# Kernel tuning notes

Measured on AMD Instinct MI355X. Metric: run time of the kernel, lower is better.

The kernel has to match this reference:

```python
import jax, jax.numpy as jnp
import numpy as np

N, E, F_IN, NUM_GRAPHS, K = 50000, 500000, 160, 128, 3


def _glorot(k, shape):
    lim = np.sqrt(6.0 / (shape[-2] + shape[-1])).astype(np.float32)
    return jax.random.uniform(k, shape, jnp.float32, -lim, lim)


def setup_inputs() -> dict:
    key = jax.random.key(0)
    ks = jax.random.split(key, 8)
    x = jax.random.normal(ks[0], (N, F_IN), jnp.float32)
    edge_index = jax.random.randint(ks[1], (2, E), 0, N)
    edge_attr = jax.random.uniform(ks[2], (E,), jnp.float32)
    batch = jnp.sort(jax.random.randint(ks[3], (N,), 0, NUM_GRAPHS))
    W1 = _glorot(ks[4], (K, F_IN, 128)); b1 = jnp.zeros((128,), jnp.float32)
    W2 = _glorot(ks[5], (K, 128, 64)); b2 = jnp.zeros((64,), jnp.float32)
    W3 = _glorot(ks[6], (K, 64, 32)); b3 = jnp.zeros((32,), jnp.float32)
    Wl = _glorot(ks[7], (32, 2)); bl = jnp.zeros((2,), jnp.float32)
    return dict(x=x, edge_index=edge_index, edge_attr=edge_attr, batch=batch,
                W1=W1, b1=b1, W2=W2, b2=b2, W3=W3, b3=b3, Wl=Wl, bl=bl)


def _cheb_norm(src, dst, edge_attr, n):
    # PyG ChebConv: sym-normalized Laplacian, lambda_max=2 =>
    # L_hat = (2/lmax)*L_sym - I = -D^{-1/2} A D^{-1/2} (diagonal = 0)
    deg = jax.ops.segment_sum(edge_attr, src, num_segments=n)
    safe = jnp.where(deg > 0, deg, 1.0)
    dinv = jnp.where(deg > 0, jax.lax.rsqrt(safe), 0.0)
    return -dinv[src] * edge_attr * dinv[dst]


def _propagate(x, src, dst, w, n):
    # out[dst] += w * x[src]  (sparse L_hat @ x)
    return jax.ops.segment_sum(w[:, None] * x[src], dst, num_segments=n)


def _cheb_conv(x, src, dst, w, W, b, n):
    # Chebyshev recurrence: T0 = x, T1 = L_hat x, Tk = 2 L_hat T(k-1) - T(k-2)
    tx0 = x
    out = tx0 @ W[0]
    tx1 = _propagate(tx0, src, dst, w, n)
    out = out + tx1 @ W[1]
    for k in range(2, W.shape[0]):
        tx2 = 2.0 * _propagate(tx1, src, dst, w, n) - tx0
        out = out + tx2 @ W[k]
        tx0, tx1 = tx1, tx2
    return out + b


def reference(x, edge_index, edge_attr, batch, W1, b1, W2, b2, W3, b3, Wl, bl):
    n = x.shape[0]
    src, dst = edge_index[0], edge_index[1]
    w = _cheb_norm(src, dst, edge_attr, n)
    h = jax.nn.relu(_cheb_conv(x, src, dst, w, W1, b1, n))
    h = jax.nn.relu(_cheb_conv(h, src, dst, w, W2, b2, n))
    h = jax.nn.relu(_cheb_conv(h, src, dst, w, W3, b3, n))
    # global_mean_pool over graph ids (dropout omitted: eval mode)
    sums = jax.ops.segment_sum(h, batch, num_segments=NUM_GRAPHS)
    cnt = jax.ops.segment_sum(jnp.ones((n,), h.dtype), batch, num_segments=NUM_GRAPHS)
    pooled = sums / jnp.maximum(cnt, 1.0)[:, None]
    return pooled @ Wl + bl
```

## Files before the change

### kernel.cpp

```cpp
#include <hip/hip_runtime.h>

#define N_NODES 50000
#define N_EDGES 500000
#define NUM_G   128
#define SCAN_NB 49
#define PN      (SCAN_NB * 1024)
#define NCX     32
#define NCX_SH  5
#define ECH     15628
#define RNG     8192
#define NRY     7
#define HVB     (2 * NCX * NRY)
#define WPREPB  360
#define RNG_SC  2688
#define NRY_SC  19
#define SCVB    (NCX * NRY_SC)
#define GEMM_MB 782

typedef __attribute__((ext_vector_type(8))) short short8;
typedef __attribute__((ext_vector_type(4))) float f32x4;
typedef __attribute__((ext_vector_type(2))) float f32x2;

__device__ __forceinline__ unsigned f2bf(float x) {
    unsigned u = __float_as_uint(x);
    return (u + 0x7FFFu + ((u >> 16) & 1u)) >> 16;
}
__device__ __forceinline__ float bf2f(unsigned h) {
    return __uint_as_float(h << 16);
}

__device__ __forceinline__ void wprep_one(const float* __restrict__ W, unsigned short* __restrict__ WT,
                                          int t, int FIN, int F) {
    int n = t / FIN, k = t - n * FIN;
    int sel = n / F, c = n - sel * F;
    float v;
    if (sel == 0) v = W[(size_t)k * F + c] - W[(size_t)2 * FIN * F + (size_t)k * F + c];
    else          v = W[(size_t)sel * FIN * F + (size_t)k * F + c];
    WT[t] = (unsigned short)f2bf(v);
}

__global__ __launch_bounds__(256)
void prep_kernel(const int* __restrict__ src, const int* __restrict__ dst,
                 const float* __restrict__ ea,
                 float* __restrict__ pdeg, int* __restrict__ pcnt,
                 const float* __restrict__ W1, const float* __restrict__ W2,
                 const float* __restrict__ W3,
                 unsigned short* __restrict__ WT1, unsigned short* __restrict__ WT2,
                 unsigned short* __restrict__ WT3) {
    __shared__ unsigned lh[RNG];
    int vb = blockIdx.x, tid = threadIdx.x;
    if (vb < HVB) {
        bool isdeg = vb < NCX * NRY;
        int v2 = isdeg ? vb : vb - NCX * NRY;
        int xk = v2 & (NCX - 1), y = v2 >> NCX_SH;
        int base = y * RNG;
        for (int i = tid; i < RNG; i += 256) lh[i] = 0u;
        __syncthreads();
        int e0 = xk * ECH, e1 = min(e0 + ECH, N_EDGES);
        if (isdeg) {
            for (int e = e0 + tid * 4; e < e1; e += 1024) {
                int4 s4 = *reinterpret_cast<const int4*>(src + e);
                if ((unsigned)(s4.x - base) < RNG) atomicAdd((float*)&lh[s4.x - base], ea[e]);
                if ((unsigned)(s4.y - base) < RNG) atomicAdd((float*)&lh[s4.y - base], ea[e + 1]);
                if ((unsigned)(s4.z - base) < RNG) atomicAdd((float*)&lh[s4.z - base], ea[e + 2]);
                if ((unsigned)(s4.w - base) < RNG) atomicAdd((float*)&lh[s4.w - base], ea[e + 3]);
            }
        } else {
            for (int e = e0 + tid * 4; e < e1; e += 1024) {
                int4 d4 = *reinterpret_cast<const int4*>(dst + e);
                if ((unsigned)(d4.x - base) < RNG) atomicAdd((int*)&lh[d4.x - base], 1);
                if ((unsigned)(d4.y - base) < RNG) atomicAdd((int*)&lh[d4.y - base], 1);
                if ((unsigned)(d4.z - base) < RNG) atomicAdd((int*)&lh[d4.z - base], 1);
                if ((unsigned)(d4.w - base) < RNG) atomicAdd((int*)&lh[d4.w - base], 1);
            }
        }
        __syncthreads();
        if (isdeg) {
            for (int i = tid; i < RNG; i += 256) {
                int n = base + i;
                if (n < PN) pdeg[(size_t)xk * PN + n] = ((float*)lh)[i];
            }
        } else {
            for (int i = tid; i < RNG; i += 256) {
                int n = base + i;
                if (n < PN) pcnt[(size_t)xk * PN + n] = ((int*)lh)[i];
            }
        }
    } else {
        int t = (vb - HVB) * 256 + tid;
        if (t < 61440)      wprep_one(W1, WT1, t, 160, 128);
        else if (t < 86016) wprep_one(W2, WT2, t - 61440, 128, 64);
        else if (t < 92160) wprep_one(W3, WT3, t - 86016, 64, 32);
    }
}

__global__ __launch_bounds__(256)
void reduce_scan_kernel(const float* __restrict__ pdeg, int* __restrict__ pcnt,
                        float* __restrict__ dinv, int* __restrict__ cnt,
                        int* __restrict__ partial) {
    int b = blockIdx.x, t = threadIdx.x;
    int i0 = b * 1024 + t * 4;
    float d0 = 0.f, d1 = 0.f, d2 = 0.f, d3 = 0.f;
    int r0 = 0, r1 = 0, r2 = 0, r3 = 0;
    for (int x = 0; x < NCX; ++x) {
        float4 pv = *reinterpret_cast<const float4*>(pdeg + (size_t)x * PN + i0);
        int4   cv = *reinterpret_cast<const int4*>(pcnt + (size_t)x * PN + i0);
        *reinterpret_cast<int4*>(pcnt + (size_t)x * PN + i0) = make_int4(r0, r1, r2, r3);
        d0 += pv.x; d1 += pv.y; d2 += pv.z; d3 += pv.w;
        r0 += cv.x; r1 += cv.y; r2 += cv.z; r3 += cv.w;
    }
    float dd[4] = {d0, d1, d2, d3};
    int   rr[4] = {r0, r1, r2, r3};
    int s = 0;
    #pragma unroll
    for (int j = 0; j < 4; ++j) {
        int n = i0 + j;
        if (n < N_NODES) {
            float dv = dd[j], r = 0.f;
            if (dv > 0.f) {
                r = rsqrtf(dv);
                r = r * (1.5f - 0.5f * dv * r * r);
            }
            dinv[n] = r;
            cnt[n] = rr[j];
            s += rr[j];
        } else {
            cnt[n] = 0;
        }
    }
    __shared__ int red[256];
    red[t] = s;
    __syncthreads();
    for (int off = 128; off > 0; off >>= 1) {
        if (t < off) red[t] += red[t + off];
        __syncthreads();
    }
    if (t == 0) partial[b] = red[0];
}

__global__ __launch_bounds__(256)
void scan_final_kernel(const int* __restrict__ cnt, const int* __restrict__ partial,
                       int* __restrict__ rowptr, int n) {
    int b = blockIdx.x, t = threadIdx.x;
    __shared__ int red[256];
    __shared__ int sh_off, sh_tot;
    if (t < 64) {
        int orig = (t < SCAN_NB) ? partial[t] : 0;
        int v = orig;
        #pragma unroll
        for (int off = 1; off < 64; off <<= 1) {
            int u = __shfl_up(v, off, 64);
            if (t >= off) v += u;
        }
        if (t == b) sh_off = v - orig;
        if (t == SCAN_NB - 1) sh_tot = v;
    }
    __syncthreads();
    int4 v = reinterpret_cast<const int4*>(cnt)[b * 256 + t];
    int s = v.x + v.y + v.z + v.w;
    red[t] = s;
    __syncthreads();
    for (int off = 1; off < 256; off <<= 1) {
        int u = (t >= off) ? red[t - off] : 0;
        __syncthreads();
        red[t] += u;
        __syncthreads();
    }
    int excl = sh_off + ((t == 0) ? 0 : red[t - 1]);
    int i0 = b * 1024 + t * 4;
    if (i0 < n)     rowptr[i0]     = excl;
    if (i0 + 1 < n) rowptr[i0 + 1] = excl + v.x;
    if (i0 + 2 < n) rowptr[i0 + 2] = excl + v.x + v.y;
    if (i0 + 3 < n) rowptr[i0 + 3] = excl + v.x + v.y + v.z;
    if (b == SCAN_NB - 1 && t == 0) rowptr[n] = sh_tot;
}

__device__ void scatter_body(int vb, const int* __restrict__ src, const int* __restrict__ dst,
                             const float* __restrict__ ea,
                             const int* __restrict__ rowptr, const int* __restrict__ pcnt,
                             int2* __restrict__ csr, unsigned char* smraw) {
    int* cursor = (int*)smraw;
    int tid = threadIdx.x;
    int x = vb & (NCX - 1), y = vb >> NCX_SH;
    int base = y * RNG_SC;
    for (int i = tid; i < RNG_SC; i += 256) {
        int n = base + i;
        cursor[i] = (n < N_NODES) ? (rowptr[n] + pcnt[(size_t)x * PN + n]) : 0;
    }
    __syncthreads();
    int e0 = x * ECH, e1 = min(e0 + ECH, N_EDGES);
    for (int e = e0 + tid * 4; e < e1; e += 1024) {
        int4 d4 = *reinterpret_cast<const int4*>(dst + e);
        if ((unsigned)(d4.x - base) < RNG_SC) {
            int pos = atomicAdd(&cursor[d4.x - base], 1);
            csr[pos] = make_int2(src[e], __float_as_int(ea[e]));
        }
        if ((unsigned)(d4.y - base) < RNG_SC) {
            int pos = atomicAdd(&cursor[d4.y - base], 1);
            csr[pos] = make_int2(src[e + 1], __float_as_int(ea[e + 1]));
        }
        if ((unsigned)(d4.z - base) < RNG_SC) {
            int pos = atomicAdd(&cursor[d4.z - base], 1);
            csr[pos] = make_int2(src[e + 2], __float_as_int(ea[e + 2]));
        }
        if ((unsigned)(d4.w - base) < RNG_SC) {
            int pos = atomicAdd(&cursor[d4.w - base], 1);
            csr[pos] = make_int2(src[e + 3], __float_as_int(ea[e + 3]));
        }
    }
}

template<int FIN, int F, bool AFP32>
__device__ void gemm_body(int bx, const void* __restrict__ Araw,
                          const unsigned short* __restrict__ WT, const float* __restrict__ dinv,
                          unsigned short* __restrict__ Y0, unsigned short* __restrict__ Y1,
                          unsigned short* __restrict__ Y2, int nrows, unsigned char* smraw) {
    constexpr int KT = FIN / 32;
    constexpr int NT = F / 32;
    constexpr int NTT = 3 * NT;
    constexpr int SA = FIN + 8;
    constexpr int F8 = FIN / 8;
    short* Bs = (short*)smraw;

    int tid = threadIdx.x;
    int lane = tid & 63, w = tid >> 6;
    int m0 = bx * 64;

    int colb = lane & 15;
    int q8 = (lane >> 4) << 3;
    int rq = (lane >> 4) << 2;
    int arow = m0 + w * 16 + colb;
    bool rok = arow < nrows;

    short8 afr[KT];
    #pragma unroll
    for (int kt = 0; kt < KT; ++kt) {
        short8 z = {0, 0, 0, 0, 0, 0, 0, 0};
        if (!rok) { afr[kt] = z; continue; }
        if constexpr (AFP32) {
            const float* A = (const float*)Araw;
            float4 f0 = *reinterpret_cast<const float4*>(A + (size_t)arow * FIN + (kt << 5) + q8);
            float4 f1 = *reinterpret_cast<const float4*>(A + (size_t)arow * FIN + (kt << 5) + q8 + 4);
            short8 r;
            r[0] = (short)f2bf(f0.x); r[1] = (short)f2bf(f0.y);
            r[2] = (short)f2bf(f0.z); r[3] = (short)f2bf(f0.w);
            r[4] = (short)f2bf(f1.x); r[5] = (short)f2bf(f1.y);
            r[6] = (short)f2bf(f1.z); r[7] = (short)f2bf(f1.w);
            afr[kt] = r;
        } else {
            const unsigned short* A = (const unsigned short*)Araw;
            afr[kt] = *reinterpret_cast<const short8*>(A + (size_t)arow * FIN + (kt << 5) + q8);
        }
    }

    for (int nt = 0; nt < NTT; ++nt) {
        int n0 = nt << 5;
        __syncthreads();
        for (int span = tid; span < 32 * F8; span += 256) {
            int r = span / F8, c8 = (span - r * F8) << 3;
            int pr = (r < 16) ? (r << 1) : (((r - 16) << 1) + 1);
            *reinterpret_cast<uint4*>(&Bs[r * SA + c8]) =
                *reinterpret_cast<const uint4*>(WT + (size_t)(n0 + pr) * FIN + c8);
        }
        __syncthreads();

        f32x4 acc0 = {0.f, 0.f, 0.f, 0.f}, acc1 = acc0;
        #pragma unroll
        for (int kt = 0; kt < KT; ++kt) {
            short8 b0 = *reinterpret_cast<const short8*>(&Bs[colb * SA + (kt << 5) + q8]);
            short8 b1 = *reinterpret_cast<const short8*>(&Bs[(colb + 16) * SA + (kt << 5) + q8]);
            acc0 = __builtin_amdgcn_mfma_f32_16x16x32_bf16(afr[kt], b0, acc0, 0, 0, 0);
            acc1 = __builtin_amdgcn_mfma_f32_16x16x32_bf16(afr[kt], b1, acc1, 0, 0, 0);
        }

        int g = nt / NT;
        int ntg = nt - g * NT;
        unsigned short* Ys = (g == 0) ? Y0 : (g == 1) ? Y1 : Y2;
        int lc = (ntg << 5) + (colb << 1);
        #pragma unroll
        for (int r = 0; r < 4; ++r) {
            int orow = m0 + w * 16 + rq + r;
            if (orow < nrows) {
                float sc = (g == 2) ? dinv[orow] : 1.0f;
                unsigned pack = f2bf(acc0[r] * sc) | (f2bf(acc1[r] * sc) << 16);
                *reinterpret_cast<unsigned*>(Ys + (size_t)orow * F + lc) = pack;
            }
        }
    }
}

__global__ __launch_bounds__(256)
void sg_kernel(const int* __restrict__ src, const int* __restrict__ dst,
               const float* __restrict__ ea,
               const int* __restrict__ rowptr, const int* __restrict__ pcnt,
               int2* __restrict__ csr,
               const float* __restrict__ x, const unsigned short* __restrict__ WT1,
               const float* __restrict__ dinv,
               unsigned short* __restrict__ Y0, unsigned short* __restrict__ Y1,
               unsigned short* __restrict__ Y2) {
    __shared__ alignas(16) unsigned char sm[32 * (160 + 8) * 2];
    int vb = blockIdx.x;
    if (vb < SCVB) {
        scatter_body(vb, src, dst, ea, rowptr, pcnt, csr, sm);
    } else {
        gemm_body<160, 128, true>(vb - SCVB, x, WT1, dinv, Y0, Y1, Y2, N_NODES, sm);
    }
}

template<int FIN, int F>
__launch_bounds__(256)
__global__ void cheb_gemm(const unsigned short* __restrict__ Xb, const unsigned short* __restrict__ WT,
                          const float* __restrict__ dinv,
                          unsigned short* __restrict__ Y0, unsigned short* __restrict__ Y1,
                          unsigned short* __restrict__ Y2, int nrows) {
    __shared__ alignas(16) unsigned char sm[32 * (FIN + 8) * 2];
    gemm_body<FIN, F, false>(blockIdx.x, Xb, WT, dinv, Y0, Y1, Y2, nrows, sm);
}

__device__ __forceinline__ void acc8p(f32x2* acc, uint4 p, float wv) {
    f32x2 w2; w2[0] = wv; w2[1] = wv;
    f32x2 a0, a1, a2, a3;
    a0[0] = __uint_as_float(p.x << 16); a0[1] = __uint_as_float(p.x & 0xFFFF0000u);
    a1[0] = __uint_as_float(p.y << 16); a1[1] = __uint_as_float(p.y & 0xFFFF0000u);
    a2[0] = __uint_as_float(p.z << 16); a2[1] = __uint_as_float(p.z & 0xFFFF0000u);
    a3[0] = __uint_as_float(p.w << 16); a3[1] = __uint_as_float(p.w & 0xFFFF0000u);
    acc[0] += w2 * a0;
    acc[1] += w2 * a1;
    acc[2] += w2 * a2;
    acc[3] += w2 * a3;
}

__device__ __forceinline__ void expand8(uint4 p, float* o) {
    o[0] = bf2f(p.x & 0xFFFFu);
    o[1] = __uint_as_float(p.x & 0xFFFF0000u);
    o[2] = bf2f(p.y & 0xFFFFu);
    o[3] = __uint_as_float(p.y & 0xFFFF0000u);
    o[4] = bf2f(p.z & 0xFFFFu);
    o[5] = __uint_as_float(p.z & 0xFFFF0000u);
    o[6] = bf2f(p.w & 0xFFFFu);
    o[7] = __uint_as_float(p.w & 0xFFFF0000u);
}

template<int F, int MODE>
__launch_bounds__(256)
__global__ void gather_kernel(const unsigned short* __restrict__ X, const int2* __restrict__ csr,
                              const int* __restrict__ rowptr, const float* __restrict__ dinv,
                              const unsigned short* __restrict__ Y, const float* __restrict__ bias,
                              unsigned short* __restrict__ O, int n) {
    constexpr int FQ8 = F >> 3;
    constexpr int DPB = 256 / FQ8;
    constexpr int CAP = 1280;
    __shared__ int2 scsr[CAP];
    __shared__ int srp[DPB + 1];
    __shared__ int smap[DPB];
    int tid = threadIdx.x;
    int db0 = blockIdx.x * DPB;
    if (tid <= DPB) srp[tid] = rowptr[min(db0 + tid, n)];
    __syncthreads();
    int ebeg = srp[0];
    int ecnt = srp[DPB] - ebeg;
    bool staged = ecnt <= CAP;
    if (tid < DPB) {
        int my = srp[tid + 1] - srp[tid];
        int rk = 0;
        for (int g2 = 0; g2 < DPB; ++g2) {
            int l2 = srp[g2 + 1] - srp[g2];
            rk += (l2 < my) || (l2 == my && g2 < tid);
        }
        smap[rk] = tid;
    }
    if (staged) {
        for (int i = tid; i < ecnt; i += 256)
            scsr[i] = csr[ebeg + i];
    }
    __syncthreads();

    int gq = tid / FQ8;
    int rr = smap[gq];
    int d = db0 + rr;
    if (d >= n) return;
    int f8 = (tid - gq * FQ8) << 3;
    f32x2 acc[4];
    #pragma unroll
    for (int j = 0; j < 4; ++j) { acc[j][0] = 0.f; acc[j][1] = 0.f; }

    if (staged) {
        int beg = srp[rr] - ebeg, end = srp[rr + 1] - ebeg;
        int last = end - 1;
        for (int i = beg; i < end; i += 8) {
            int2 e0 = scsr[i];
            int2 e1 = scsr[min(i + 1, last)];
            int2 e2 = scsr[min(i + 2, last)];
            int2 e3 = scsr[min(i + 3, last)];
            int2 e4 = scsr[min(i + 4, last)];
            int2 e5 = scsr[min(i + 5, last)];
            int2 e6 = scsr[min(i + 6, last)];
            int2 e7 = scsr[min(i + 7, last)];
            uint4 p0 = *reinterpret_cast<const uint4*>(X + (size_t)e0.x * F + f8);
            uint4 p1 = *reinterpret_cast<const uint4*>(X + (size_t)e1.x * F + f8);
            uint4 p2 = *reinterpret_cast<const uint4*>(X + (size_t)e2.x * F + f8);
            uint4 p3 = *reinterpret_cast<const uint4*>(X + (size_t)e3.x * F + f8);
            uint4 p4 = *reinterpret_cast<const uint4*>(X + (size_t)e4.x * F + f8);
            uint4 p5 = *reinterpret_cast<const uint4*>(X + (size_t)e5.x * F + f8);
            uint4 p6 = *reinterpret_cast<const uint4*>(X + (size_t)e6.x * F + f8);
            uint4 p7 = *reinterpret_cast<const uint4*>(X + (size_t)e7.x * F + f8);
            float w0 = __int_as_float(e0.y);
            float w1 = (i + 1 < end) ? __int_as_float(e1.y) : 0.f;
            float w2 = (i + 2 < end) ? __int_as_float(e2.y) : 0.f;
            float w3 = (i + 3 < end) ? __int_as_float(e3.y) : 0.f;
            float w4 = (i + 4 < end) ? __int_as_float(e4.y) : 0.f;
            float w5 = (i + 5 < end) ? __int_as_float(e5.y) : 0.f;
            float w6 = (i + 6 < end) ? __int_as_float(e6.y) : 0.f;
            float w7 = (i + 7 < end) ? __int_as_float(e7.y) : 0.f;
            acc8p(acc, p0, w0);
            acc8p(acc, p1, w1);
            acc8p(acc, p2, w2);
            acc8p(acc, p3, w3);
            acc8p(acc, p4, w4);
            acc8p(acc, p5, w5);
            acc8p(acc, p6, w6);
            acc8p(acc, p7, w7);
        }
    } else {
        int beg = srp[rr], end = srp[rr + 1];
        for (int i = beg; i < end; ++i) {
            int2 e = csr[i];
            uint4 p = *reinterpret_cast<const uint4*>(X + (size_t)e.x * F + f8);
            acc8p(acc, p, __int_as_float(e.y));
        }
    }

    float accs[8];
    #pragma unroll
    for (int j = 0; j < 8; ++j) accs[j] = acc[j >> 1][j & 1];

    float y[8];
    expand8(*reinterpret_cast<const uint4*>(Y + (size_t)d * F + f8), y);
    float dv = dinv[d];
    float v[8];
    if (MODE == 0) {
        float dv2 = 2.f * dv;
        #pragma unroll
        for (int j = 0; j < 8; ++j) v[j] = dv * (y[j] - dv2 * accs[j]);
    } else {
        float4 ba = *reinterpret_cast<const float4*>(bias + f8);
        float4 bb = *reinterpret_cast<const float4*>(bias + f8 + 4);
        v[0] = fmaxf(y[0] - dv * accs[0] + ba.x, 0.f);
        v[1] = fmaxf(y[1] - dv * accs[1] + ba.y, 0.f);
        v[2] = fmaxf(y[2] - dv * accs[2] + ba.z, 0.f);
        v[3] = fmaxf(y[3] - dv * accs[3] + ba.w, 0.f);
        v[4] = fmaxf(y[4] - dv * accs[4] + bb.x, 0.f);
        v[5] = fmaxf(y[5] - dv * accs[5] + bb.y, 0.f);
        v[6] = fmaxf(y[6] - dv * accs[6] + bb.z, 0.f);
        v[7] = fmaxf(y[7] - dv * accs[7] + bb.w, 0.f);
    }
    uint4 o;
    o.x = f2bf(v[0]) | (f2bf(v[1]) << 16);
    o.y = f2bf(v[2]) | (f2bf(v[3]) << 16);
    o.z = f2bf(v[4]) | (f2bf(v[5]) << 16);
    o.w = f2bf(v[6]) | (f2bf(v[7]) << 16);
    *reinterpret_cast<uint4*>(O + (size_t)d * F + f8) = o;
}

__device__ __forceinline__ int lower_bound_dev(const int* __restrict__ a, int n, int v) {
    int lo = 0, hi = n;
    while (lo < hi) {
        int mid = (lo + hi) >> 1;
        if (a[mid] < v) lo = mid + 1; else hi = mid;
    }
    return lo;
}

__global__ void pool_kernel(const unsigned short* __restrict__ H, const int* __restrict__ batch,
                            const float* __restrict__ Wl, const float* __restrict__ bl,
                            float* __restrict__ out, int n) {
    int g = blockIdx.x;
    int start = lower_bound_dev(batch, n, g);
    int end   = lower_bound_dev(batch, n, g + 1);
    int tid = threadIdx.x;
    int f = tid & 31;
    int sub = tid >> 5;
    float acc = 0.0f;
    for (int i = start + sub; i < end; i += 8)
        acc += bf2f((unsigned)H[(size_t)i * 32 + f]);
    __shared__ float red[256];
    red[tid] = acc;
    __syncthreads();
    if (tid < 128) red[tid] += red[tid + 128];
    __syncthreads();
    if (tid < 64) red[tid] += red[tid + 64];
    __syncthreads();
    if (tid < 32) red[tid] += red[tid + 32];
    __syncthreads();
    if (tid < 2) {
        int cnt = end - start;
        float inv = 1.0f / (float)(cnt > 0 ? cnt : 1);
        float o = bl[tid];
        for (int f2 = 0; f2 < 32; ++f2)
            o += red[f2] * inv * Wl[f2 * 2 + tid];
        out[g * 2 + tid] = o;
    }
}

extern "C" void kernel_launch(void* const* d_in, const int* in_sizes, int n_in,
                              void* d_out, int out_size, void* d_ws, size_t ws_size,
                              hipStream_t stream) {
    const float* x     = (const float*)d_in[0];
    const int*   ei    = (const int*)d_in[1];
    const float* ea    = (const float*)d_in[2];
    const int*   batch = (const int*)d_in[3];
    const float* W1 = (const float*)d_in[4];
    const float* b1 = (const float*)d_in[5];
    const float* W2 = (const float*)d_in[6];
    const float* b2 = (const float*)d_in[7];
    const float* W3 = (const float*)d_in[8];
    const float* b3 = (const float*)d_in[9];
    const float* Wl = (const float*)d_in[10];
    const float* bl = (const float*)d_in[11];
    float* out = (float*)d_out;
    char* ws = (char*)d_ws;

    const int* src = ei;
    const int* dst = ei + N_EDGES;

    size_t off = 0;
    auto alloc = [&](size_t bytes) { char* p = ws + off; off += (bytes + 255) & ~(size_t)255; return p; };
    float* pdeg    = (float*)alloc((size_t)NCX * PN * 4);
    int*   pcnt    = (int*)  alloc((size_t)NCX * PN * 4);
    float* dinv    = (float*)alloc(N_NODES * 4);
    int*   cnt     = (int*)  alloc((size_t)PN * 4);
    int*   partial = (int*)  alloc(SCAN_NB * 4);
    int*   rowptr  = (int*)  alloc((N_NODES + 1) * 4);
    int2*  csr     = (int2*) alloc((size_t)N_EDGES * 8);
    unsigned short* Xb  = (unsigned short*)alloc((size_t)N_NODES * 160 * 2);
    unsigned short* Y0  = (unsigned short*)alloc((size_t)N_NODES * 128 * 2);
    unsigned short* Y1  = (unsigned short*)alloc((size_t)N_NODES * 128 * 2);
    unsigned short* Y2  = (unsigned short*)alloc((size_t)N_NODES * 128 * 2);
    unsigned short* U   = (unsigned short*)alloc((size_t)N_NODES * 128 * 2);
    unsigned short* WT1 = (unsigned short*)alloc((size_t)384 * 160 * 2);
    unsigned short* WT2 = (unsigned short*)alloc((size_t)192 * 128 * 2);
    unsigned short* WT3 = (unsigned short*)alloc((size_t)96 * 64 * 2);

    const int BT = 256;

    prep_kernel<<<HVB + WPREPB, BT, 0, stream>>>(src, dst, ea, pdeg, pcnt,
                                                 W1, W2, W3, WT1, WT2, WT3);
    reduce_scan_kernel<<<SCAN_NB, BT, 0, stream>>>(pdeg, pcnt, dinv, cnt, partial);
    scan_final_kernel<<<SCAN_NB, BT, 0, stream>>>(cnt, partial, rowptr, N_NODES);
    sg_kernel<<<SCVB + GEMM_MB, BT, 0, stream>>>(src, dst, ea, rowptr, pcnt, csr,
                                                 x, WT1, dinv, Y0, Y1, Y2);

    auto gb = [&](int F) { int DPB = 256 / (F / 8); return (N_NODES + DPB - 1) / DPB; };

    gather_kernel<128, 0><<<gb(128), BT, 0, stream>>>(Y2, csr, rowptr, dinv, Y1, nullptr, U, N_NODES);
    gather_kernel<128, 1><<<gb(128), BT, 0, stream>>>(U, csr, rowptr, dinv, Y0, b1, Xb, N_NODES);

    cheb_gemm<128, 64><<<GEMM_MB, BT, 0, stream>>>(Xb, WT2, dinv, Y0, Y1, Y2, N_NODES);
    gather_kernel<64, 0><<<gb(64), BT, 0, stream>>>(Y2, csr, rowptr, dinv, Y1, nullptr, U, N_NODES);
    gather_kernel<64, 1><<<gb(64), BT, 0, stream>>>(U, csr, rowptr, dinv, Y0, b2, Xb, N_NODES);

    cheb_gemm<64, 32><<<GEMM_MB, BT, 0, stream>>>(Xb, WT3, dinv, Y0, Y1, Y2, N_NODES);
    gather_kernel<32, 0><<<gb(32), BT, 0, stream>>>(Y2, csr, rowptr, dinv, Y1, nullptr, U, N_NODES);
    gather_kernel<32, 1><<<gb(32), BT, 0, stream>>>(U, csr, rowptr, dinv, Y0, b3, Xb, N_NODES);

    pool_kernel<<<NUM_G, BT, 0, stream>>>(Xb, batch, Wl, bl, out, N_NODES);
}
```

Baseline: 288.8 us.

## Split each destination row's edge list across two thread groups in gather kernel

The gather kernel now assigns two thread groups per destination node, each summing half of that node's incoming edges. The partial sums are combined through shared memory after a block barrier, and the staged CSR capacity shrinks to match the halved nodes per block. The aim is more memory-level parallelism and shorter per-thread dependency chains on the random row loads, at the cost of an extra barrier, shared-memory traffic and twice as many blocks. The histogram range and per-block count constants in the prep stage are also retuned.

```diff
diff --git a/kernel.cpp b/kernel.cpp
--- a/kernel.cpp
+++ b/kernel.cpp
@@ -8,8 +8,8 @@
 #define NCX     32
 #define NCX_SH  5
 #define ECH     15628
-#define RNG     8192
-#define NRY     7
+#define RNG     15360
+#define NRY     4
 #define HVB     (2 * NCX * NRY)
 #define WPREPB  360
 #define RNG_SC  2688
@@ -348,11 +348,13 @@
                               const unsigned short* __restrict__ Y, const float* __restrict__ bias,
                               unsigned short* __restrict__ O, int n) {
     constexpr int FQ8 = F >> 3;
-    constexpr int DPB = 256 / FQ8;
-    constexpr int CAP = 1280;
+    constexpr int TPR = 2 * FQ8;
+    constexpr int DPB = 256 / TPR;
+    constexpr int CAP = 768;
     __shared__ int2 scsr[CAP];
     __shared__ int srp[DPB + 1];
     __shared__ int smap[DPB];
+    __shared__ float comb[DPB * F];
     int tid = threadIdx.x;
     int db0 = blockIdx.x * DPB;
     if (tid <= DPB) srp[tid] = rowptr[min(db0 + tid, n)];
@@ -375,64 +377,82 @@
     }
     __syncthreads();
 
-    int gq = tid / FQ8;
+    int gq = tid / TPR;
+    int q  = tid - gq * TPR;
+    int sub = q / FQ8;
+    int fidx = q - sub * FQ8;
     int rr = smap[gq];
     int d = db0 + rr;
-    if (d >= n) return;
-    int f8 = (tid - gq * FQ8) << 3;
+    bool act = d < n;
+    int f8 = fidx << 3;
     f32x2 acc[4];
     #pragma unroll
     for (int j = 0; j < 4; ++j) { acc[j][0] = 0.f; acc[j][1] = 0.f; }
 
-    if (staged) {
-        int beg = srp[rr] - ebeg, end = srp[rr + 1] - ebeg;
-        int last = end - 1;
-        for (int i = beg; i < end; i += 8) {
-            int2 e0 = scsr[i];
-            int2 e1 = scsr[min(i + 1, last)];
-            int2 e2 = scsr[min(i + 2, last)];
-            int2 e3 = scsr[min(i + 3, last)];
-            int2 e4 = scsr[min(i + 4, last)];
-            int2 e5 = scsr[min(i + 5, last)];
-            int2 e6 = scsr[min(i + 6, last)];
-            int2 e7 = scsr[min(i + 7, last)];
-            uint4 p0 = *reinterpret_cast<const uint4*>(X + (size_t)e0.x * F + f8);
-            uint4 p1 = *reinterpret_cast<const uint4*>(X + (size_t)e1.x * F + f8);
-            uint4 p2 = *reinterpret_cast<const uint4*>(X + (size_t)e2.x * F + f8);
-            uint4 p3 = *reinterpret_cast<const uint4*>(X + (size_t)e3.x * F + f8);
-            uint4 p4 = *reinterpret_cast<const uint4*>(X + (size_t)e4.x * F + f8);
-            uint4 p5 = *reinterpret_cast<const uint4*>(X + (size_t)e5.x * F + f8);
-            uint4 p6 = *reinterpret_cast<const uint4*>(X + (size_t)e6.x * F + f8);
-            uint4 p7 = *reinterpret_cast<const uint4*>(X + (size_t)e7.x * F + f8);
-            float w0 = __int_as_float(e0.y);
-            float w1 = (i + 1 < end) ? __int_as_float(e1.y) : 0.f;
-            float w2 = (i + 2 < end) ? __int_as_float(e2.y) : 0.f;
-            float w3 = (i + 3 < end) ? __int_as_float(e3.y) : 0.f;
-            float w4 = (i + 4 < end) ? __int_as_float(e4.y) : 0.f;
-            float w5 = (i + 5 < end) ? __int_as_float(e5.y) : 0.f;
-            float w6 = (i + 6 < end) ? __int_as_float(e6.y) : 0.f;
-            float w7 = (i + 7 < end) ? __int_as_float(e7.y) : 0.f;
-            acc8p(acc, p0, w0);
-            acc8p(acc, p1, w1);
-            acc8p(acc, p2, w2);
-            acc8p(acc, p3, w3);
-            acc8p(acc, p4, w4);
-            acc8p(acc, p5, w5);
-            acc8p(acc, p6, w6);
-            acc8p(acc, p7, w7);
-        }
-    } else {
-        int beg = srp[rr], end = srp[rr + 1];
-        for (int i = beg; i < end; ++i) {
-            int2 e = csr[i];
-            uint4 p = *reinterpret_cast<const uint4*>(X + (size_t)e.x * F + f8);
-            acc8p(acc, p, __int_as_float(e.y));
-        }
-    }
+    if (act) {
+        if (staged) {
+            int begR = srp[rr] - ebeg, endR = srp[rr + 1] - ebeg;
+            int mid = begR + ((endR - begR + 1) >> 1);
+            int beg = sub ? mid : begR;
+            int end = sub ? endR : mid;
+            int last = end - 1;
+            for (int i = beg; i < end; i += 8) {
+                int2 e0 = scsr[i];
+                int2 e1 = scsr[min(i + 1, last)];
+                int2 e2 = scsr[min(i + 2, last)];
+                int2 e3 = scsr[min(i + 3, last)];
+                int2 e4 = scsr[min(i + 4, last)];
+                int2 e5 = scsr[min(i + 5, last)];
+                int2 e6 = scsr[min(i + 6, last)];
+                int2 e7 = scsr[min(i + 7, last)];
+                uint4 p0 = *reinterpret_cast<const uint4*>(X + (size_t)e0.x * F + f8);
+                uint4 p1 = *reinterpret_cast<const uint4*>(X + (size_t)e1.x * F + f8);
+                uint4 p2 = *reinterpret_cast<const uint4*>(X + (size_t)e2.x * F + f8);
+                uint4 p3 = *reinterpret_cast<const uint4*>(X + (size_t)e3.x * F + f8);
+                uint4 p4 = *reinterpret_cast<const uint4*>(X + (size_t)e4.x * F + f8);
+                uint4 p5 = *reinterpret_cast<const uint4*>(X + (size_t)e5.x * F + f8);
+                uint4 p6 = *reinterpret_cast<const uint4*>(X + (size_t)e6.x * F + f8);
+                uint4 p7 = *reinterpret_cast<const uint4*>(X + (size_t)e7.x * F + f8);
+                float w0 = __int_as_float(e0.y);
+                float w1 = (i + 1 < end) ? __int_as_float(e1.y) : 0.f;
+                float w2 = (i + 2 < end) ? __int_as_float(e2.y) : 0.f;
+                float w3 = (i + 3 < end) ? __int_as_float(e3.y) : 0.f;
+                float w4 = (i + 4 < end) ? __int_as_float(e4.y) : 0.f;
+                float w5 = (i + 5 < end) ? __int_as_float(e5.y) : 0.f;
+                float w6 = (i + 6 < end) ? __int_as_float(e6.y) : 0.f;
+                float w7 = (i + 7 < end) ? __int_as_float(e7.y) : 0.f;
+                acc8p(acc, p0, w0);
+                acc8p(acc, p1, w1);
+                acc8p(acc, p2, w2);
+                acc8p(acc, p3, w3);
+                acc8p(acc, p4, w4);
+                acc8p(acc, p5, w5);
+                acc8p(acc, p6, w6);
+                acc8p(acc, p7, w7);
+            }
+        } else {
+            int begR = srp[rr], endR = srp[rr + 1];
+            int mid = begR + ((endR - begR + 1) >> 1);
+            int beg = sub ? mid : begR;
+            int end = sub ? endR : mid;
+            for (int i = beg; i < end; ++i) {
+                int2 e = csr[i];
+                uint4 p = *reinterpret_cast<const uint4*>(X + (size_t)e.x * F + f8);
+                acc8p(acc, p, __int_as_float(e.y));
+            }
+        }
+    }
+
+    if (act && sub == 1) {
+        #pragma unroll
+        for (int j = 0; j < 8; ++j) comb[gq * F + f8 + j] = acc[j >> 1][j & 1];
+    }
+    __syncthreads();
+    if (!act || sub == 1) return;
 
     float accs[8];
     #pragma unroll
-    for (int j = 0; j < 8; ++j) accs[j] = acc[j >> 1][j & 1];
+    for (int j = 0; j < 8; ++j) accs[j] = acc[j >> 1][j & 1] + comb[gq * F + f8 + j];
 
     float y[8];
     expand8(*reinterpret_cast<const uint4*>(Y + (size_t)d * F + f8), y);
@@ -550,7 +570,7 @@
     sg_kernel<<<SCVB + GEMM_MB, BT, 0, stream>>>(src, dst, ea, rowptr, pcnt, csr,
                                                  x, WT1, dinv, Y0, Y1, Y2);
 
-    auto gb = [&](int F) { int DPB = 256 / (F / 8); return (N_NODES + DPB - 1) / DPB; };
+    auto gb = [&](int F) { int DPB = 1024 / F; return (N_NODES + DPB - 1) / DPB; };
 
     gather_kernel<128, 0><<<gb(128), BT, 0, stream>>>(Y2, csr, rowptr, dinv, Y1, nullptr, U, N_NODES);
     gather_kernel<128, 1><<<gb(128), BT, 0, stream>>>(U, csr, rowptr, dinv, Y0, b1, Xb, N_NODES);
```

Result: slower. 296.4 us (+2.6%).
